# Kernel optimization log

Measured on AMD Instinct MI355X. Metric: run time of the kernel, lower is better.

## Reference

```python
import jax, jax.numpy as jnp
import numpy as np

N_NODES = 100000


def _add_self_loops(edge_index, n):
    loop = jnp.arange(n, dtype=edge_index.dtype)
    src = jnp.concatenate([edge_index[0], loop])
    dst = jnp.concatenate([edge_index[1], loop])
    return src, dst


def _gcn_conv(x, W, b, src, dst, n):
    # h = X W, then symmetric-normalized scatter-add over edges (PyG GCNConv)
    h = x @ W
    ones = jnp.ones(src.shape[0], dtype=h.dtype)
    deg = jax.ops.segment_sum(ones, dst, num_segments=n)  # in-degree incl. self loops
    dinv = jnp.where(deg > 0, jax.lax.rsqrt(deg), 0.0)
    norm = dinv[src] * dinv[dst]                           # [E]
    msg = h[src] * norm[:, None]                           # gather + scale
    out = jax.ops.segment_sum(msg, dst, num_segments=n)    # scatter-add
    return out + b


def setup_inputs() -> dict:
    key = jax.random.key(0)
    k1, k2, k3, k4 = jax.random.split(key, 4)
    F, H, C = 128, 128, 16
    x = jax.random.normal(k1, (N_NODES, F), dtype=jnp.float32)
    edge_index = jax.random.randint(k2, (2, 1600000), 0, N_NODES, dtype=jnp.int64)
    W1 = jax.random.normal(k3, (F, H), dtype=jnp.float32) / np.sqrt(F)
    b1 = jnp.zeros((H,), dtype=jnp.float32)
    W2 = jax.random.normal(k4, (H, C), dtype=jnp.float32) / np.sqrt(H)
    b2 = jnp.zeros((C,), dtype=jnp.float32)
    return {"x": x, "edge_index": edge_index, "W1": W1, "b1": b1, "W2": W2, "b2": b2}


def reference(x, edge_index, W1, b1, W2, b2):
    n = x.shape[0]
    src, dst = _add_self_loops(edge_index, n)
    h = _gcn_conv(x, W1, b1, src, dst, n)
    h = jax.nn.relu(h)
    # dropout(p=0.1) treated as identity (deterministic eval-mode reference)
    logits = _gcn_conv(h, W2, b2, src, dst, n)
    return logits, jax.nn.log_softmax(logits, axis=1)
```

## Files before the change

### kernel.cpp

```cpp
#include <hip/hip_runtime.h>
#include <math.h>


#define ELLW 72
#define EPB 16384
#define BSH 9
#define MAXEB 100
#define MAXBK 200
#define SORTCAP 10240

typedef __attribute__((ext_vector_type(8))) short short8;
typedef __attribute__((ext_vector_type(4))) float f32x4;
typedef __attribute__((ext_vector_type(4))) int i32x4;
typedef __attribute__((ext_vector_type(4))) _Float16 f16x4;

__device__ __forceinline__ float bf2f(unsigned short u) {
    return __uint_as_float(((unsigned int)u) << 16);
}
__device__ __forceinline__ unsigned short f2bf(float f) {
    unsigned int u = __float_as_uint(f);
    unsigned int r = (u + 0x7fffu + ((u >> 16) & 1u)) >> 16;
    return (unsigned short)r;
}
__device__ __forceinline__ f32x4 h2f4(f16x4 v) {
    f32x4 r;
    r[0] = (float)v[0]; r[1] = (float)v[1]; r[2] = (float)v[2]; r[3] = (float)v[3];
    return r;
}

__global__ void k_prep_hist(unsigned short* __restrict__ h, _Float16* __restrict__ g,
                            const float* __restrict__ W1, unsigned short* __restrict__ wt,
                            int n, const int* __restrict__ dst, int E,
                            int* __restrict__ hist, int nbuck, float* __restrict__ dinv) {
    __shared__ int lh[MAXBK];
    const int t = threadIdx.x;
    if (blockIdx.x < 64) {
        int i = blockIdx.x * 256 + t;
        if (i < 16384) {
            int nc = i >> 7, k = i & 127;
            wt[i] = f2bf(W1[k * 128 + nc]);
        }
        if (i < 128) h[(size_t)n * 128 + i] = 0;
        if (i < 16) g[(size_t)n * 16 + i] = (_Float16)0.f;
        if (i < 1) dinv[n] = 1.f;
        return;
    }
    const int blk = blockIdx.x - 64;
    for (int i = t; i < nbuck; i += 256) lh[i] = 0;
    __syncthreads();
    const int e0 = blk * EPB;
    const int e1 = min(e0 + EPB, E);
    for (int e = e0 + t; e < e1; e += 256)
        atomicAdd(&lh[dst[e] >> BSH], 1);
    __syncthreads();
    for (int i = t; i < nbuck; i += 256)
        hist[blk * nbuck + i] = lh[i];
}

__global__ void k_scan(int* __restrict__ hist, int* __restrict__ bstart,
                       int* __restrict__ bcount, int neb, int nbuck) {
    __shared__ unsigned short lh[MAXEB * MAXBK];
    __shared__ int sc[256];
    const int t = threadIdx.x;
    const int items = neb * nbuck;
    const int it4 = items >> 2;
    for (int i = t; i < it4; i += 256) {
        i32x4 v = *(const i32x4*)(hist + i * 4);
        lh[i * 4 + 0] = (unsigned short)v[0];
        lh[i * 4 + 1] = (unsigned short)v[1];
        lh[i * 4 + 2] = (unsigned short)v[2];
        lh[i * 4 + 3] = (unsigned short)v[3];
    }
    for (int i = (it4 << 2) + t; i < items; i += 256)
        lh[i] = (unsigned short)hist[i];
    __syncthreads();
    int total = 0;
    if (t < nbuck)
        for (int blk = 0; blk < neb; ++blk) total += lh[blk * nbuck + t];
    sc[t] = total;
    __syncthreads();
    for (int o = 1; o < 256; o <<= 1) {
        int x = 0;
        if (t >= o) x = sc[t - o];
        __syncthreads();
        if (t >= o) sc[t] += x;
        __syncthreads();
    }
    if (t < nbuck) {
        int run = sc[t] - total;
        bstart[t] = run;
        bcount[t] = total;
        for (int blk = 0; blk < neb; ++blk) {
            int idx = blk * nbuck + t;
            int v = lh[idx];
            hist[idx] = run;
            run += v;
        }
    }
}

__global__ __launch_bounds__(256) void k_bin_gemm(
        const int* __restrict__ src, const int* __restrict__ dst, int E,
        const int* __restrict__ hist, int* __restrict__ binned, int nbuck, int neb,
        const float* __restrict__ x, const unsigned short* __restrict__ wt,
        unsigned short* __restrict__ h, int n) {
    __shared__ unsigned short xs[64 * 136];
    const int t = threadIdx.x;
    if ((int)blockIdx.x < neb) {
        int* cnt = (int*)xs;
        const int blk = blockIdx.x;
        for (int i = t; i < nbuck; i += 256) cnt[i] = hist[blk * nbuck + i];
        __syncthreads();
        const int e0 = blk * EPB;
        const int e1 = min(e0 + EPB, E);
        for (int e = e0 + t; e < e1; e += 256) {
            int d = dst[e];
            int b = d >> BSH;
            int pos = atomicAdd(&cnt[b], 1);
            binned[pos] = src[e] | ((d & ((1 << BSH) - 1)) << 17);
        }
        return;
    }
    const int row0 = ((int)blockIdx.x - neb) * 64;
    for (int i = t; i < 2048; i += 256) {
        int r = i >> 5, c4 = (i & 31) << 2;
        int gr = row0 + r;
        float4 v = make_float4(0.f, 0.f, 0.f, 0.f);
        if (gr < n) v = *(const float4*)(x + (size_t)gr * 128 + c4);
        ushort4 u;
        u.x = f2bf(v.x); u.y = f2bf(v.y); u.z = f2bf(v.z); u.w = f2bf(v.w);
        *(ushort4*)(xs + r * 136 + c4) = u;
    }
    __syncthreads();
    const int w = t >> 6;
    const int lane = t & 63;
    const int m = lane & 15, q = lane >> 4;
    f32x4 acc[8];
#pragma unroll
    for (int ns = 0; ns < 8; ++ns) acc[ns] = (f32x4){0.f, 0.f, 0.f, 0.f};
#pragma unroll
    for (int kt = 0; kt < 4; ++kt) {
        short8 a = *(const short8*)(xs + (w * 16 + m) * 136 + kt * 32 + q * 8);
#pragma unroll
        for (int ns = 0; ns < 8; ++ns) {
            short8 b = *(const short8*)((const short*)wt + (ns * 16 + m) * 128 + kt * 32 + q * 8);
            acc[ns] = __builtin_amdgcn_mfma_f32_16x16x32_bf16(a, b, acc[ns], 0, 0, 0);
        }
    }
    unsigned short* xsw = xs + (w * 16) * 136;
#pragma unroll
    for (int ns = 0; ns < 8; ++ns)
#pragma unroll
        for (int reg = 0; reg < 4; ++reg)
            xsw[(q * 4 + reg) * 136 + ns * 16 + m] = f2bf(acc[ns][reg]);
    __syncthreads();
#pragma unroll
    for (int it = 0; it < 8; ++it) {
        int rl = (lane >> 5) + it * 2;
        int off = (lane & 31) * 4;
        int gr = row0 + w * 16 + rl;
        if (gr < n)
            *(ushort4*)(h + (size_t)gr * 128 + off) = *(const ushort4*)(xsw + rl * 136 + off);
    }
}

__global__ __launch_bounds__(256) void k_ell(
        const int* __restrict__ binned, const int* __restrict__ bstart,
        const int* __restrict__ bcount, int* __restrict__ deg,
        float* __restrict__ dinv, int* __restrict__ col, int n) {
    __shared__ int sorted[SORTCAP];
    __shared__ int ldeg[1 << BSH];
    __shared__ int off[1 << BSH];
    __shared__ int cur[1 << BSH];
    __shared__ int psum[256];
    const int t = threadIdx.x, b = blockIdx.x;
    const int node0 = b << BSH;
    const int st = bstart[b], cv = bcount[b];
    for (int i = t; i < (1 << BSH); i += 256) { ldeg[i] = 0; cur[i] = 0; }
    __syncthreads();
    for (int i = t; i < cv; i += 256)
        atomicAdd(&ldeg[binned[st + i] >> 17], 1);
    __syncthreads();

    if (cv <= SORTCAP) {
        int c0 = min(ldeg[2 * t], ELLW);
        int c1 = min(ldeg[2 * t + 1], ELLW);
        psum[t] = c0 + c1;
        __syncthreads();
        for (int o = 1; o < 256; o <<= 1) {
            int v = 0;
            if (t >= o) v = psum[t - o];
            __syncthreads();
            psum[t] += v;
            __syncthreads();
        }
        int base = psum[t] - (c0 + c1);
        off[2 * t] = base;
        off[2 * t + 1] = base + c0;
        __syncthreads();
        for (int i = t; i < cv; i += 256) {
            int v = binned[st + i];
            int dl = v >> 17;
            int r = atomicAdd(&cur[dl], 1);
            if (r < ELLW) sorted[off[dl] + r] = v & 0x1FFFF;
        }
        __syncthreads();
        const int nn = min(1 << BSH, n - node0);
        const int totv = nn * (ELLW / 4);
        int* colb = col + (size_t)node0 * ELLW;
        for (int idx = t; idx < totv; idx += 256) {
            int i = idx / (ELLW / 4);
            int q = (idx - i * (ELLW / 4)) * 4;
            int dc = min(ldeg[i], ELLW);
            int o = off[i];
            i32x4 v;
#pragma unroll
            for (int j = 0; j < 4; ++j)
                v[j] = (q + j < dc) ? sorted[o + q + j] : n;
            *(i32x4*)(colb + (size_t)i * ELLW + q) = v;
        }
    } else {
        for (int i = t; i < cv; i += 256) {
            int v = binned[st + i];
            int s = v & 0x1FFFF;
            int dl = v >> 17;
            int r = atomicAdd(&cur[dl], 1);
            if (r < ELLW) col[(size_t)(node0 + dl) * ELLW + r] = s;
        }
        __syncthreads();
        for (int i = t; i < (1 << BSH); i += 256) {
            int node = node0 + i;
            if (node < n) {
                int dc = min(ldeg[i], ELLW);
                int kend = (dc + 7) & ~7;
                for (int q = dc; q < kend; ++q) col[(size_t)node * ELLW + q] = n;
            }
        }
    }
    for (int i = t; i < (1 << BSH); i += 256) {
        int node = node0 + i;
        if (node < n) {
            int dgv = ldeg[i];
            deg[node] = dgv;
            dinv[node] = rsqrtf((float)(min(dgv, ELLW) + 1));
        }
    }
}

__global__ __launch_bounds__(256, 2) void k_gather1f(
        const unsigned short* __restrict__ h, const int* __restrict__ deg,
        const float* __restrict__ dinv, const int* __restrict__ col,
        const float* __restrict__ b1, const float* __restrict__ W2,
        _Float16* __restrict__ g, int n) {
    const int t = threadIdx.x;
    const int lane = t & 15;
    const int d = blockIdx.x * 16 + (t >> 4);
    if (d >= n) return;
    int dg = deg[d];
    if (dg > ELLW) dg = ELLW;
    const float dd = dinv[d];
    const int kend = (dg + 7) & ~7;
    const int* ecol = col + (size_t)d * ELLW;

    float aA[8], aB[8];
    {
        short8 u = *(const short8*)(h + (size_t)d * 128 + lane * 8);
#pragma unroll
        for (int j = 0; j < 8; ++j) {
            aA[j] = dd * bf2f((unsigned short)u[j]);
            aB[j] = 0.f;
        }
    }
    for (int k = 0; k < kend; k += 8) {
        int4 c0 = *(const int4*)(ecol + k);
        int4 c1 = *(const int4*)(ecol + k + 4);
        float e0 = dinv[c0.x], e1 = dinv[c0.y], e2 = dinv[c0.z], e3 = dinv[c0.w];
        float e4 = dinv[c1.x], e5 = dinv[c1.y], e6 = dinv[c1.z], e7 = dinv[c1.w];
        short8 u0 = *(const short8*)(h + (size_t)c0.x * 128 + lane * 8);
        short8 u1 = *(const short8*)(h + (size_t)c0.y * 128 + lane * 8);
        short8 u2 = *(const short8*)(h + (size_t)c0.z * 128 + lane * 8);
        short8 u3 = *(const short8*)(h + (size_t)c0.w * 128 + lane * 8);
        short8 u4 = *(const short8*)(h + (size_t)c1.x * 128 + lane * 8);
        short8 u5 = *(const short8*)(h + (size_t)c1.y * 128 + lane * 8);
        short8 u6 = *(const short8*)(h + (size_t)c1.z * 128 + lane * 8);
        short8 u7 = *(const short8*)(h + (size_t)c1.w * 128 + lane * 8);
#pragma unroll
        for (int j = 0; j < 8; ++j) {
            aA[j] = fmaf(bf2f((unsigned short)u0[j]), e0, aA[j]);
            aB[j] = fmaf(bf2f((unsigned short)u1[j]), e1, aB[j]);
            aA[j] = fmaf(bf2f((unsigned short)u2[j]), e2, aA[j]);
            aB[j] = fmaf(bf2f((unsigned short)u3[j]), e3, aB[j]);
            aA[j] = fmaf(bf2f((unsigned short)u4[j]), e4, aA[j]);
            aB[j] = fmaf(bf2f((unsigned short)u5[j]), e5, aB[j]);
            aA[j] = fmaf(bf2f((unsigned short)u6[j]), e6, aA[j]);
            aB[j] = fmaf(bf2f((unsigned short)u7[j]), e7, aB[j]);
        }
    }
    float y[8];
    const float* b1p = b1 + lane * 8;
#pragma unroll
    for (int j = 0; j < 8; ++j)
        y[j] = fmaxf(fmaf(aA[j] + aB[j], dd, b1p[j]), 0.f);
    const float4* w2v = (const float4*)(W2 + lane * 8 * 16);
    float4 z0 = make_float4(0.f, 0.f, 0.f, 0.f);
    float4 z1 = z0, z2 = z0, z3 = z0;
#pragma unroll
    for (int j = 0; j < 8; ++j) {
        float4 w0 = w2v[j * 4 + 0], w1 = w2v[j * 4 + 1];
        float4 w2 = w2v[j * 4 + 2], w3 = w2v[j * 4 + 3];
        float yj = y[j];
        z0.x = fmaf(yj, w0.x, z0.x); z0.y = fmaf(yj, w0.y, z0.y);
        z0.z = fmaf(yj, w0.z, z0.z); z0.w = fmaf(yj, w0.w, z0.w);
        z1.x = fmaf(yj, w1.x, z1.x); z1.y = fmaf(yj, w1.y, z1.y);
        z1.z = fmaf(yj, w1.z, z1.z); z1.w = fmaf(yj, w1.w, z1.w);
        z2.x = fmaf(yj, w2.x, z2.x); z2.y = fmaf(yj, w2.y, z2.y);
        z2.z = fmaf(yj, w2.z, z2.z); z2.w = fmaf(yj, w2.w, z2.w);
        z3.x = fmaf(yj, w3.x, z3.x); z3.y = fmaf(yj, w3.y, z3.y);
        z3.z = fmaf(yj, w3.z, z3.z); z3.w = fmaf(yj, w3.w, z3.w);
    }
#pragma unroll
    for (int mm = 1; mm < 16; mm <<= 1) {
        z0.x += __shfl_xor(z0.x, mm); z0.y += __shfl_xor(z0.y, mm);
        z0.z += __shfl_xor(z0.z, mm); z0.w += __shfl_xor(z0.w, mm);
        z1.x += __shfl_xor(z1.x, mm); z1.y += __shfl_xor(z1.y, mm);
        z1.z += __shfl_xor(z1.z, mm); z1.w += __shfl_xor(z1.w, mm);
        z2.x += __shfl_xor(z2.x, mm); z2.y += __shfl_xor(z2.y, mm);
        z2.z += __shfl_xor(z2.z, mm); z2.w += __shfl_xor(z2.w, mm);
        z3.x += __shfl_xor(z3.x, mm); z3.y += __shfl_xor(z3.y, mm);
        z3.z += __shfl_xor(z3.z, mm); z3.w += __shfl_xor(z3.w, mm);
    }
    if (lane < 4) {
        float4 z = (lane == 0) ? z0 : (lane == 1) ? z1 : (lane == 2) ? z2 : z3;
        f16x4 zz;
        zz[0] = (_Float16)(z.x * dd); zz[1] = (_Float16)(z.y * dd);
        zz[2] = (_Float16)(z.z * dd); zz[3] = (_Float16)(z.w * dd);
        *(f16x4*)(g + (size_t)d * 16 + lane * 4) = zz;
    }
}

__global__ void k_gather2(const _Float16* __restrict__ g, const int* __restrict__ deg,
                          const int* __restrict__ col, const float* __restrict__ b2,
                          float* __restrict__ out, int n) {
    const int t = threadIdx.x;
    const int d = blockIdx.x * 64 + (t >> 2);
    if (d >= n) return;
    const int l = t & 3;
    int dg = deg[d];
    if (dg > ELLW) dg = ELLW;
    const float dd = rsqrtf((float)(dg + 1));
    const int kend = (dg + 7) & ~7;
    const int* ecol = col + (size_t)d * ELLW;
    const _Float16* gl = g + l * 4;

    f32x4 aA = h2f4(*(const f16x4*)(gl + (size_t)d * 16));
    f32x4 aB = (f32x4){0.f, 0.f, 0.f, 0.f};
    f32x4 aC = aB, aD = aB;
    for (int k = 0; k < kend; k += 8) {
        int4 c0 = *(const int4*)(ecol + k);
        int4 c1 = *(const int4*)(ecol + k + 4);
        f16x4 h0 = *(const f16x4*)(gl + (size_t)c0.x * 16);
        f16x4 h1 = *(const f16x4*)(gl + (size_t)c0.y * 16);
        f16x4 h2 = *(const f16x4*)(gl + (size_t)c0.z * 16);
        f16x4 h3 = *(const f16x4*)(gl + (size_t)c0.w * 16);
        f16x4 h4 = *(const f16x4*)(gl + (size_t)c1.x * 16);
        f16x4 h5 = *(const f16x4*)(gl + (size_t)c1.y * 16);
        f16x4 h6 = *(const f16x4*)(gl + (size_t)c1.z * 16);
        f16x4 h7 = *(const f16x4*)(gl + (size_t)c1.w * 16);
        aA += h2f4(h0); aB += h2f4(h1); aC += h2f4(h2); aD += h2f4(h3);
        aA += h2f4(h4); aB += h2f4(h5); aC += h2f4(h6); aD += h2f4(h7);
    }
    f32x4 bv = *(const f32x4*)(b2 + l * 4);
    f32x4 acc = (aA + aB + aC + aD) * dd + bv;
    *(f32x4*)(out + (size_t)d * 16 + l * 4) = acc;
    float m = fmaxf(fmaxf(acc[0], acc[1]), fmaxf(acc[2], acc[3]));
    m = fmaxf(m, __shfl_xor(m, 1));
    m = fmaxf(m, __shfl_xor(m, 2));
    float e = expf(acc[0] - m) + expf(acc[1] - m) + expf(acc[2] - m) + expf(acc[3] - m);
    e += __shfl_xor(e, 1);
    e += __shfl_xor(e, 2);
    float ls = m + logf(e);
    f32x4 o;
    o[0] = acc[0] - ls; o[1] = acc[1] - ls; o[2] = acc[2] - ls; o[3] = acc[3] - ls;
    *(f32x4*)(out + (size_t)n * 16 + (size_t)d * 16 + l * 4) = o;
}

static inline size_t align256(size_t v) { return (v + 255) & ~(size_t)255; }

extern "C" void kernel_launch(void* const* d_in, const int* in_sizes, int n_in,
                              void* d_out, int out_size, void* d_ws, size_t ws_size,
                              hipStream_t stream) {
    const float* x  = (const float*)d_in[0];
    const int*   ei = (const int*)d_in[1];
    const float* W1 = (const float*)d_in[2];
    const float* b1 = (const float*)d_in[3];
    const float* W2 = (const float*)d_in[4];
    const float* b2 = (const float*)d_in[5];
    float* out = (float*)d_out;

    const int n = in_sizes[0] / 128;
    const int E = in_sizes[1] / 2;
    const int* src = ei;
    const int* dst = ei + E;
    const int NEB = (E + EPB - 1) / EPB;
    const int NBUCK = (n + (1 << BSH) - 1) >> BSH;

    char* base = (char*)d_ws;
    size_t off = 0;
    int* deg = (int*)(base + off); off = align256(off + (size_t)n * 4);
    float* dinv = (float*)(base + off); off = align256(off + ((size_t)n + 1) * 4);
    int* col = (int*)(base + off); off = align256(off + (size_t)n * ELLW * 4);
    unsigned short* wt = (unsigned short*)(base + off); off = align256(off + 128 * 128 * 2);
    unsigned short* h = (unsigned short*)(base + off); off = align256(off + ((size_t)n + 1) * 128 * 2);
    _Float16* g = (_Float16*)(base + off); off = align256(off + ((size_t)n + 1) * 16 * 2);
    int* hist = (int*)(base + off); off = align256(off + (size_t)MAXEB * MAXBK * 4);
    int* bstart = (int*)(base + off); off = align256(off + (size_t)MAXBK * 4);
    int* bcount = (int*)(base + off); off = align256(off + (size_t)MAXBK * 4);
    int* binned = (int*)(base + off); off = align256(off + (size_t)E * 4);

    k_prep_hist<<<64 + NEB, 256, 0, stream>>>(h, g, W1, wt, n, dst, E, hist, NBUCK, dinv);
    k_scan<<<1, 256, 0, stream>>>(hist, bstart, bcount, NEB, NBUCK);
    k_bin_gemm<<<NEB + (n + 63) / 64, 256, 0, stream>>>(
        src, dst, E, hist, binned, NBUCK, NEB, x, wt, h, n);
    k_ell<<<NBUCK, 256, 0, stream>>>(binned, bstart, bcount, deg, dinv, col, n);

    k_gather1f<<<(n + 15) / 16, 256, 0, stream>>>(h, deg, dinv, col, b1, W2, g, n);

    k_gather2<<<(n + 63) / 64, 256, 0, stream>>>(g, deg, col, b2, out, n);
}
```

Baseline: 344.1 us.

## Parallelize bucket scan across blocks and widen gather2 loads to 8 halfs

Replaces the single-block k_scan with a per-bucket column-scan kernel (one block per bucket) and recomputes the bucket-start exclusive scan redundantly inside k_bin_gemm and k_ell, removing a serial single-block bottleneck and the bstart buffer. Separately, k_gather2 now uses 2 lanes per node with 16-byte f16x8 gathers instead of 4 lanes with 8-byte loads, halving load instructions per edge. This adds redundant small scans to every binning and ELL block, and the column scan assumes NEB is at most 128.

```diff
diff --git a/kernel.cpp b/kernel.cpp
--- a/kernel.cpp
+++ b/kernel.cpp
@@ -13,6 +13,7 @@
 typedef __attribute__((ext_vector_type(4))) float f32x4;
 typedef __attribute__((ext_vector_type(4))) int i32x4;
 typedef __attribute__((ext_vector_type(4))) _Float16 f16x4;
+typedef __attribute__((ext_vector_type(8))) _Float16 f16x8;
 
 __device__ __forceinline__ float bf2f(unsigned short u) {
     return __uint_as_float(((unsigned int)u) << 16);
@@ -21,11 +22,6 @@
     unsigned int u = __float_as_uint(f);
     unsigned int r = (u + 0x7fffu + ((u >> 16) & 1u)) >> 16;
     return (unsigned short)r;
-}
-__device__ __forceinline__ f32x4 h2f4(f16x4 v) {
-    f32x4 r;
-    r[0] = (float)v[0]; r[1] = (float)v[1]; r[2] = (float)v[2]; r[3] = (float)v[3];
-    return r;
 }
 
 __global__ void k_prep_hist(unsigned short* __restrict__ h, _Float16* __restrict__ g,
@@ -57,59 +53,54 @@
         hist[blk * nbuck + i] = lh[i];
 }
 
-__global__ void k_scan(int* __restrict__ hist, int* __restrict__ bstart,
-                       int* __restrict__ bcount, int neb, int nbuck) {
-    __shared__ unsigned short lh[MAXEB * MAXBK];
-    __shared__ int sc[256];
-    const int t = threadIdx.x;
-    const int items = neb * nbuck;
-    const int it4 = items >> 2;
-    for (int i = t; i < it4; i += 256) {
-        i32x4 v = *(const i32x4*)(hist + i * 4);
-        lh[i * 4 + 0] = (unsigned short)v[0];
-        lh[i * 4 + 1] = (unsigned short)v[1];
-        lh[i * 4 + 2] = (unsigned short)v[2];
-        lh[i * 4 + 3] = (unsigned short)v[3];
-    }
-    for (int i = (it4 << 2) + t; i < items; i += 256)
-        lh[i] = (unsigned short)hist[i];
-    __syncthreads();
-    int total = 0;
-    if (t < nbuck)
-        for (int blk = 0; blk < neb; ++blk) total += lh[blk * nbuck + t];
-    sc[t] = total;
-    __syncthreads();
-    for (int o = 1; o < 256; o <<= 1) {
-        int x = 0;
-        if (t >= o) x = sc[t - o];
-        __syncthreads();
-        if (t >= o) sc[t] += x;
-        __syncthreads();
-    }
-    if (t < nbuck) {
-        int run = sc[t] - total;
-        bstart[t] = run;
-        bcount[t] = total;
-        for (int blk = 0; blk < neb; ++blk) {
-            int idx = blk * nbuck + t;
-            int v = lh[idx];
-            hist[idx] = run;
-            run += v;
-        }
-    }
+__global__ __launch_bounds__(128) void k_colsum(int* __restrict__ hist,
+                                                int* __restrict__ bcount,
+                                                int neb, int nbuck) {
+    __shared__ int v[128];
+    __shared__ int p[128];
+    const int t = threadIdx.x, b = blockIdx.x;
+    int x = 0;
+    if (t < neb) x = hist[t * nbuck + b];
+    v[t] = x;
+    p[t] = x;
+    __syncthreads();
+    for (int o = 1; o < 128; o <<= 1) {
+        int y = 0;
+        if (t >= o) y = p[t - o];
+        __syncthreads();
+        p[t] += y;
+        __syncthreads();
+    }
+    if (t < neb) hist[t * nbuck + b] = p[t] - v[t];
+    if (t == 127) bcount[b] = p[127];
 }
 
 __global__ __launch_bounds__(256) void k_bin_gemm(
         const int* __restrict__ src, const int* __restrict__ dst, int E,
-        const int* __restrict__ hist, int* __restrict__ binned, int nbuck, int neb,
+        const int* __restrict__ hist, const int* __restrict__ bcount,
+        int* __restrict__ binned, int nbuck, int neb,
         const float* __restrict__ x, const unsigned short* __restrict__ wt,
         unsigned short* __restrict__ h, int n) {
     __shared__ unsigned short xs[64 * 136];
     const int t = threadIdx.x;
     if ((int)blockIdx.x < neb) {
         int* cnt = (int*)xs;
+        int* ps  = ((int*)xs) + MAXBK;
+        int* ex  = ((int*)xs) + MAXBK + 256;
         const int blk = blockIdx.x;
-        for (int i = t; i < nbuck; i += 256) cnt[i] = hist[blk * nbuck + i];
+        int myc = (t < nbuck) ? bcount[t] : 0;
+        ps[t] = myc;
+        __syncthreads();
+        for (int o = 1; o < 256; o <<= 1) {
+            int y = 0;
+            if (t >= o) y = ps[t - o];
+            __syncthreads();
+            ps[t] += y;
+            __syncthreads();
+        }
+        ex[t] = ps[t] - myc;
+        __syncthreads();
+        if (t < nbuck) cnt[t] = ex[t] + hist[blk * nbuck + t];
         __syncthreads();
         const int e0 = blk * EPB;
         const int e1 = min(e0 + EPB, E);
@@ -165,19 +156,31 @@
 }
 
 __global__ __launch_bounds__(256) void k_ell(
-        const int* __restrict__ binned, const int* __restrict__ bstart,
-        const int* __restrict__ bcount, int* __restrict__ deg,
-        float* __restrict__ dinv, int* __restrict__ col, int n) {
+        const int* __restrict__ binned, const int* __restrict__ bcount,
+        int* __restrict__ deg, float* __restrict__ dinv, int* __restrict__ col,
+        int n, int nbuck) {
     __shared__ int sorted[SORTCAP];
     __shared__ int ldeg[1 << BSH];
     __shared__ int off[1 << BSH];
     __shared__ int cur[1 << BSH];
     __shared__ int psum[256];
+    __shared__ int s_st, s_cv;
     const int t = threadIdx.x, b = blockIdx.x;
     const int node0 = b << BSH;
-    const int st = bstart[b], cv = bcount[b];
+    int myc = (t < nbuck) ? bcount[t] : 0;
+    psum[t] = myc;
+    __syncthreads();
+    for (int o = 1; o < 256; o <<= 1) {
+        int y = 0;
+        if (t >= o) y = psum[t - o];
+        __syncthreads();
+        psum[t] += y;
+        __syncthreads();
+    }
+    if (t == b) { s_st = psum[b] - myc; s_cv = myc; }
     for (int i = t; i < (1 << BSH); i += 256) { ldeg[i] = 0; cur[i] = 0; }
     __syncthreads();
+    const int st = s_st, cv = s_cv;
     for (int i = t; i < cv; i += 256)
         atomicAdd(&ldeg[binned[st + i] >> 17], 1);
     __syncthreads();
@@ -342,46 +345,62 @@
                           const int* __restrict__ col, const float* __restrict__ b2,
                           float* __restrict__ out, int n) {
     const int t = threadIdx.x;
-    const int d = blockIdx.x * 64 + (t >> 2);
+    const int d = blockIdx.x * 128 + (t >> 1);
     if (d >= n) return;
-    const int l = t & 3;
+    const int l = t & 1;
     int dg = deg[d];
     if (dg > ELLW) dg = ELLW;
     const float dd = rsqrtf((float)(dg + 1));
     const int kend = (dg + 7) & ~7;
     const int* ecol = col + (size_t)d * ELLW;
-    const _Float16* gl = g + l * 4;
-
-    f32x4 aA = h2f4(*(const f16x4*)(gl + (size_t)d * 16));
-    f32x4 aB = (f32x4){0.f, 0.f, 0.f, 0.f};
-    f32x4 aC = aB, aD = aB;
+    const _Float16* gl = g + l * 8;
+
+    float aA[8], aB[8];
+    {
+        f16x8 s = *(const f16x8*)(gl + (size_t)d * 16);
+#pragma unroll
+        for (int j = 0; j < 8; ++j) { aA[j] = (float)s[j]; aB[j] = 0.f; }
+    }
     for (int k = 0; k < kend; k += 8) {
         int4 c0 = *(const int4*)(ecol + k);
         int4 c1 = *(const int4*)(ecol + k + 4);
-        f16x4 h0 = *(const f16x4*)(gl + (size_t)c0.x * 16);
-        f16x4 h1 = *(const f16x4*)(gl + (size_t)c0.y * 16);
-        f16x4 h2 = *(const f16x4*)(gl + (size_t)c0.z * 16);
-        f16x4 h3 = *(const f16x4*)(gl + (size_t)c0.w * 16);
-        f16x4 h4 = *(const f16x4*)(gl + (size_t)c1.x * 16);
-        f16x4 h5 = *(const f16x4*)(gl + (size_t)c1.y * 16);
-        f16x4 h6 = *(const f16x4*)(gl + (size_t)c1.z * 16);
-        f16x4 h7 = *(const f16x4*)(gl + (size_t)c1.w * 16);
-        aA += h2f4(h0); aB += h2f4(h1); aC += h2f4(h2); aD += h2f4(h3);
-        aA += h2f4(h4); aB += h2f4(h5); aC += h2f4(h6); aD += h2f4(h7);
-    }
-    f32x4 bv = *(const f32x4*)(b2 + l * 4);
-    f32x4 acc = (aA + aB + aC + aD) * dd + bv;
-    *(f32x4*)(out + (size_t)d * 16 + l * 4) = acc;
-    float m = fmaxf(fmaxf(acc[0], acc[1]), fmaxf(acc[2], acc[3]));
+        f16x8 u0 = *(const f16x8*)(gl + (size_t)c0.x * 16);
+        f16x8 u1 = *(const f16x8*)(gl + (size_t)c0.y * 16);
+        f16x8 u2 = *(const f16x8*)(gl + (size_t)c0.z * 16);
+        f16x8 u3 = *(const f16x8*)(gl + (size_t)c0.w * 16);
+        f16x8 u4 = *(const f16x8*)(gl + (size_t)c1.x * 16);
+        f16x8 u5 = *(const f16x8*)(gl + (size_t)c1.y * 16);
+        f16x8 u6 = *(const f16x8*)(gl + (size_t)c1.z * 16);
+        f16x8 u7 = *(const f16x8*)(gl + (size_t)c1.w * 16);
+#pragma unroll
+        for (int j = 0; j < 8; ++j) {
+            aA[j] += (float)u0[j] + (float)u2[j] + (float)u4[j] + (float)u6[j];
+            aB[j] += (float)u1[j] + (float)u3[j] + (float)u5[j] + (float)u7[j];
+        }
+    }
+    float acc[8];
+    const float* b2p = b2 + l * 8;
+#pragma unroll
+    for (int j = 0; j < 8; ++j) acc[j] = fmaf(aA[j] + aB[j], dd, b2p[j]);
+    f32x4 o0 = {acc[0], acc[1], acc[2], acc[3]};
+    f32x4 o1 = {acc[4], acc[5], acc[6], acc[7]};
+    *(f32x4*)(out + (size_t)d * 16 + l * 8) = o0;
+    *(f32x4*)(out + (size_t)d * 16 + l * 8 + 4) = o1;
+    float m = acc[0];
+#pragma unroll
+    for (int j = 1; j < 8; ++j) m = fmaxf(m, acc[j]);
     m = fmaxf(m, __shfl_xor(m, 1));
-    m = fmaxf(m, __shfl_xor(m, 2));
-    float e = expf(acc[0] - m) + expf(acc[1] - m) + expf(acc[2] - m) + expf(acc[3] - m);
+    float e = 0.f;
+#pragma unroll
+    for (int j = 0; j < 8; ++j) e += expf(acc[j] - m);
     e += __shfl_xor(e, 1);
-    e += __shfl_xor(e, 2);
     float ls = m + logf(e);
-    f32x4 o;
-    o[0] = acc[0] - ls; o[1] = acc[1] - ls; o[2] = acc[2] - ls; o[3] = acc[3] - ls;
-    *(f32x4*)(out + (size_t)n * 16 + (size_t)d * 16 + l * 4) = o;
+    f32x4 p0, p1;
+#pragma unroll
+    for (int j = 0; j < 4; ++j) { p0[j] = acc[j] - ls; p1[j] = acc[j + 4] - ls; }
+    float* ob = out + (size_t)n * 16 + (size_t)d * 16 + l * 8;
+    *(f32x4*)(ob) = p0;
+    *(f32x4*)(ob + 4) = p1;
 }
 
 static inline size_t align256(size_t v) { return (v + 255) & ~(size_t)255; }
@@ -413,17 +432,16 @@
     unsigned short* h = (unsigned short*)(base + off); off = align256(off + ((size_t)n + 1) * 128 * 2);
     _Float16* g = (_Float16*)(base + off); off = align256(off + ((size_t)n + 1) * 16 * 2);
     int* hist = (int*)(base + off); off = align256(off + (size_t)MAXEB * MAXBK * 4);
-    int* bstart = (int*)(base + off); off = align256(off + (size_t)MAXBK * 4);
     int* bcount = (int*)(base + off); off = align256(off + (size_t)MAXBK * 4);
     int* binned = (int*)(base + off); off = align256(off + (size_t)E * 4);
 
     k_prep_hist<<<64 + NEB, 256, 0, stream>>>(h, g, W1, wt, n, dst, E, hist, NBUCK, dinv);
-    k_scan<<<1, 256, 0, stream>>>(hist, bstart, bcount, NEB, NBUCK);
+    k_colsum<<<NBUCK, 128, 0, stream>>>(hist, bcount, NEB, NBUCK);
     k_bin_gemm<<<NEB + (n + 63) / 64, 256, 0, stream>>>(
-        src, dst, E, hist, binned, NBUCK, NEB, x, wt, h, n);
-    k_ell<<<NBUCK, 256, 0, stream>>>(binned, bstart, bcount, deg, dinv, col, n);
+        src, dst, E, hist, bcount, binned, NBUCK, NEB, x, wt, h, n);
+    k_ell<<<NBUCK, 256, 0, stream>>>(binned, bcount, deg, dinv, col, n, NBUCK);
 
     k_gather1f<<<(n + 15) / 16, 256, 0, stream>>>(h, deg, dinv, col, b1, W2, g, n);
 
-    k_gather2<<<(n + 63) / 64, 256, 0, stream>>>(g, deg, col, b2, out, n);
-}
+    k_gather2<<<(n + 127) / 128, 256, 0, stream>>>(g, deg, col, b2, out, n);
+}
```

Result: no change. 346.1 us (+0.6%).
